# Performance work log

Measured on AMD Instinct MI355X. Metric: run time of the kernel, lower is better.

## Reference

```python
import jax, jax.numpy as jnp
import numpy as np

N_NODES = 100000
N_EDGES = 1600000
IN_CH, EDGE_DIM, HIDDEN, OUT_CH = 3, 3, 64, 1


def setup_inputs() -> dict:
    key = jax.random.key(0)
    ks = jax.random.split(key, 10)
    x = jax.random.normal(ks[0], (N_NODES, IN_CH), dtype=jnp.float32)
    edge_index = jax.random.randint(ks[1], (2, N_EDGES), 0, N_NODES, dtype=jnp.int64)
    edge_attr = jax.random.normal(ks[2], (N_EDGES, EDGE_DIM), dtype=jnp.float32)
    # Linear params (torch Linear: y = x @ W.T + b); we store W as (in, out)
    s1 = 1.0 / np.sqrt(IN_CH + EDGE_DIM)
    W1 = jax.random.uniform(ks[3], (IN_CH + EDGE_DIM, HIDDEN), jnp.float32, -s1, s1)
    b1 = jax.random.uniform(ks[4], (HIDDEN,), jnp.float32, -s1, s1)
    s2 = 1.0 / np.sqrt(HIDDEN + EDGE_DIM)
    W2 = jax.random.uniform(ks[5], (HIDDEN + EDGE_DIM, HIDDEN), jnp.float32, -s2, s2)
    b2 = jax.random.uniform(ks[6], (HIDDEN,), jnp.float32, -s2, s2)
    s3 = 1.0 / np.sqrt(HIDDEN)
    W3 = jax.random.uniform(ks[7], (HIDDEN, OUT_CH), jnp.float32, -s3, s3)
    b3 = jax.random.uniform(ks[8], (OUT_CH,), jnp.float32, -s3, s3)
    return {"x": x, "edge_index": edge_index, "edge_attr": edge_attr,
            "W1": W1, "b1": b1, "W2": W2, "b2": b2, "W3": W3, "b3": b3}


def _edge_conv(h, src, dst, edge_attr, W, b, n_nodes):
    # gather source node features, concat edge_attr, linear, scatter-add at dst
    msg = jnp.concatenate([h[src], edge_attr], axis=-1) @ W + b  # [E, out]
    return jax.ops.segment_sum(msg, dst, num_segments=n_nodes)   # [N, out]


def reference(x, edge_index, edge_attr, W1, b1, W2, b2, W3, b3):
    src, dst = edge_index[0], edge_index[1]  # PyG source_to_target: aggregate at edge_index[1]
    n = x.shape[0]
    h = jax.nn.relu(_edge_conv(x, src, dst, edge_attr, W1, b1, n))
    h = jax.nn.relu(_edge_conv(h, src, dst, edge_attr, W2, b2, n))
    return h @ W3 + b3  # (n_nodes, 1) anomaly logits
```

## Files before the change

kernel.cpp:

```cpp
#include <hip/hip_runtime.h>

#define N_NODES 100000
#define N_EDGES 1600000
#define NCHUNK 256
#define CHUNK_E (N_EDGES / NCHUNK)
#define BSHIFT 6
#define BMASK 63
#define NBUCK 1563
#define REC_CAP 1536


typedef unsigned int uint4_ev __attribute__((ext_vector_type(4)));
typedef short bf16x8 __attribute__((ext_vector_type(8)));
typedef float f32x4 __attribute__((ext_vector_type(4)));

__device__ __forceinline__ unsigned short f2bf(float f) {
    unsigned int u = __float_as_uint(f);
    unsigned int r = (u + 0x7fff + ((u >> 16) & 1)) >> 16;
    return (unsigned short)r;
}
__device__ __forceinline__ unsigned int pack2bf(float a, float b) {
    return (unsigned int)f2bf(a) | ((unsigned int)f2bf(b) << 16);
}
__device__ __forceinline__ float bflo(unsigned int v) { return __uint_as_float(v << 16); }
__device__ __forceinline__ float bfhi(unsigned int v) { return __uint_as_float(v & 0xffff0000u); }

__device__ __forceinline__ float4 nt_load4(const float4* p) {
    uint4_ev v = __builtin_nontemporal_load((const uint4_ev*)p);
    return make_float4(__uint_as_float(v.x), __uint_as_float(v.y),
                       __uint_as_float(v.z), __uint_as_float(v.w));
}

__device__ __forceinline__ int wave_incl_scan(int v, int lane) {
#pragma unroll
    for (int off = 1; off < 64; off <<= 1) {
        int t = __shfl_up(v, off, 64);
        if (lane >= off) v += t;
    }
    return v;
}

__global__ __launch_bounds__(1024) void k_hist(const int* __restrict__ ei,
                                               int* __restrict__ tbl,
                                               const float* __restrict__ W2,
                                               unsigned short* __restrict__ wpk,
                                               const float* __restrict__ x,
                                               float4* __restrict__ xp) {
    if (blockIdx.x > NCHUNK) {
        int i = (blockIdx.x - NCHUNK - 1) * 1024 + threadIdx.x;
        if (i < N_NODES)
            xp[i] = make_float4(x[i * 3 + 0], x[i * 3 + 1], x[i * 3 + 2], 0.f);
        return;
    }
    if (blockIdx.x == NCHUNK) {
        int i = threadIdx.x;
        if (i < 512) {
            int lane = i & 63, hh = (i >> 6) & 1, nt = i >> 7;
            int col = nt * 16 + (lane & 15);
            int k0 = hh * 32 + (lane >> 4) * 8;
#pragma unroll
            for (int j = 0; j < 8; j++)
                wpk[i * 8 + j] = f2bf(W2[(k0 + j) * 64 + col]);
        }
        return;
    }
    __shared__ int h[NBUCK];
    for (int i = threadIdx.x; i < NBUCK; i += 1024) h[i] = 0;
    __syncthreads();
    const int base = blockIdx.x * CHUNK_E;
    for (int i = threadIdx.x; i < CHUNK_E; i += 1024)
        atomicAdd(&h[ei[N_EDGES + base + i] >> BSHIFT], 1);
    __syncthreads();
    for (int i = threadIdx.x; i < NBUCK; i += 1024)
        tbl[blockIdx.x * NBUCK + i] = h[i];
}

__global__ __launch_bounds__(256) void k_colscan(int* __restrict__ tbl,
                                                 int* __restrict__ bsum) {
    const int b = blockIdx.x, t = threadIdx.x;
    int v = tbl[t * NBUCK + b];
    int lane = t & 63, w = t >> 6;
    int inc = wave_incl_scan(v, lane);
    __shared__ int ws[4];
    if (lane == 63) ws[w] = inc;
    __syncthreads();
    int wo = 0;
    for (int k = 0; k < w; k++) wo += ws[k];
    tbl[t * NBUCK + b] = wo + inc - v;
    if (t == 255) bsum[b] = wo + inc;
}

__global__ __launch_bounds__(1024) void k_basescan(const int* __restrict__ bsum,
                                                   int* __restrict__ bbase) {
    int t = threadIdx.x, lane = t & 63, w = t >> 6;
    int i0 = 2 * t, i1 = 2 * t + 1;
    int v0 = (i0 < NBUCK) ? bsum[i0] : 0;
    int v1 = (i1 < NBUCK) ? bsum[i1] : 0;
    int s = v0 + v1;
    int inc = wave_incl_scan(s, lane);
    __shared__ int ws[16];
    if (lane == 63) ws[w] = inc;
    __syncthreads();
    int wo = 0;
    for (int k = 0; k < w; k++) wo += ws[k];
    int excl = wo + inc - s;
    if (i0 < NBUCK) bbase[i0] = excl;
    if (i1 < NBUCK) bbase[i1] = excl + v0;
    if (i0 == NBUCK - 1) bbase[NBUCK] = excl + v0;
}

__global__ __launch_bounds__(1024) void k_scatter(const int* __restrict__ ei,
                                                  const float* __restrict__ ea,
                                                  const int* __restrict__ tbl,
                                                  const int* __restrict__ bbase,
                                                  float4* __restrict__ stg) {
    __shared__ int cur[NBUCK];
    for (int i = threadIdx.x; i < NBUCK; i += 1024)
        cur[i] = tbl[blockIdx.x * NBUCK + i] + bbase[i];
    __syncthreads();
    const int base = blockIdx.x * CHUNK_E;
    for (int i = threadIdx.x; i < CHUNK_E; i += 1024) {
        int e = base + i;
        int src = ei[e];
        int dst = ei[N_EDGES + e];
        float a0 = ea[(size_t)e * 3 + 0];
        float a1 = ea[(size_t)e * 3 + 1];
        float a2 = ea[(size_t)e * 3 + 2];
        int p = atomicAdd(&cur[dst >> BSHIFT], 1);
        unsigned pk = (unsigned)src | ((unsigned)(dst & BMASK) << 17);
        stg[p] = make_float4(__uint_as_float(pk), a0, a1, a2);
    }
}

__global__ __launch_bounds__(256) void k_finalize(
    const float4* __restrict__ stg, const int* __restrict__ bbase,
    const float4* __restrict__ xp, const float* __restrict__ W1,
    const float* __restrict__ b1, const float* __restrict__ W2,
    const float* __restrict__ b2, const bf16x8* __restrict__ wpk,
    int* __restrict__ csr, int* __restrict__ degp, int* __restrict__ rowend,
    unsigned int* __restrict__ zu, unsigned int* __restrict__ eu) {
    __shared__ float4 rec[REC_CAP];
    __shared__ int hist[64], lofs[64], cur[64];
    __shared__ float sU[64 * 3], sT[64 * 3];
    const int b = blockIdx.x, t = threadIdx.x;
    const int base = bbase[b], cnt = bbase[b + 1] - base;
    if (t < 64) hist[t] = 0;
    __syncthreads();
    const float* stgf = (const float*)stg;
    for (int i = t; i < cnt; i += 256) {
        unsigned pk = __float_as_uint(stgf[(size_t)(base + i) * 4]);
        atomicAdd(&hist[pk >> 17], 1);
    }
    __syncthreads();
    if (t < 64) {
        int v = hist[t];
        int inc = wave_incl_scan(v, t);
        lofs[t] = inc - v;
        cur[t] = inc - v;
    }
    __syncthreads();
    for (int i = t; i < cnt; i += 256) {
        float4 r = nt_load4(&stg[base + i]);
        unsigned pk = __float_as_uint(r.x);
        int p = atomicAdd(&cur[pk >> 17], 1);
        if (p < REC_CAP) rec[p] = r;
    }
    __syncthreads();
    {
        const int l = t >> 2, sub = t & 3;
        const int n = b * 64 + l;
        const int d = hist[l], lo = lofs[l];
        float u0 = 0, u1 = 0, u2 = 0, t0 = 0, t1 = 0, t2 = 0;
        for (int j = sub; j < d; j += 4) {
            float4 r = rec[lo + j];
            unsigned pk = __float_as_uint(r.x);
            int src = pk & 0x1FFFF;
            csr[base + lo + j] = src;
            t0 += r.y; t1 += r.z; t2 += r.w;
            float4 xv = xp[src];
            u0 += xv.x; u1 += xv.y; u2 += xv.z;
        }
#pragma unroll
        for (int off = 1; off <= 2; off <<= 1) {
            u0 += __shfl_xor(u0, off, 64); u1 += __shfl_xor(u1, off, 64);
            u2 += __shfl_xor(u2, off, 64); t0 += __shfl_xor(t0, off, 64);
            t1 += __shfl_xor(t1, off, 64); t2 += __shfl_xor(t2, off, 64);
        }
        if (sub == 0) {
            sU[l * 3 + 0] = u0; sU[l * 3 + 1] = u1; sU[l * 3 + 2] = u2;
            sT[l * 3 + 0] = t0; sT[l * 3 + 1] = t1; sT[l * 3 + 2] = t2;
            if (n < N_NODES) {
                degp[n] = d;
                rowend[n] = base + lo + d;
            }
        }
    }
    __syncthreads();
    const int lane = t & 63, w = t >> 6;
    const int tb = b * 64 + w * 16;
    if (tb >= N_NODES) return;
    const int col = lane & 15;
    const int q = lane >> 4;
    const int ln = w * 16 + col;
    const float d = (float)hist[ln];
    const float u0 = sU[ln * 3], u1 = sU[ln * 3 + 1], u2 = sU[ln * 3 + 2];
    const float t0 = sT[ln * 3], t1 = sT[ln * 3 + 1], t2 = sT[ln * 3 + 2];
    bf16x8 af[2];
#pragma unroll
    for (int h = 0; h < 2; h++) {
#pragma unroll
        for (int j = 0; j < 8; j++) {
            int c = h * 32 + q * 8 + j;
            float a = d * b1[c];
            a = fmaf(u0, W1[0 * 64 + c], a);
            a = fmaf(u1, W1[1 * 64 + c], a);
            a = fmaf(u2, W1[2 * 64 + c], a);
            a = fmaf(t0, W1[3 * 64 + c], a);
            a = fmaf(t1, W1[4 * 64 + c], a);
            a = fmaf(t2, W1[5 * 64 + c], a);
            af[h][j] = (short)f2bf(fmaxf(a, 0.f));
        }
    }
    f32x4 acc[4];
#pragma unroll
    for (int nt = 0; nt < 4; nt++) {
        bf16x8 b0 = wpk[(nt * 2 + 0) * 64 + lane];
        bf16x8 b1f = wpk[(nt * 2 + 1) * 64 + lane];
        f32x4 a = {0.f, 0.f, 0.f, 0.f};
        a = __builtin_amdgcn_mfma_f32_16x16x32_bf16(af[0], b0, a, 0, 0, 0);
        a = __builtin_amdgcn_mfma_f32_16x16x32_bf16(af[1], b1f, a, 0, 0, 0);
        acc[nt] = a;
    }
#pragma unroll
    for (int nt = 0; nt < 4; nt++) {
#pragma unroll
        for (int r = 0; r < 4; r++) {
            float v = acc[nt][r];
            float pv = __shfl_xor(v, 1, 64);
            if ((lane & 1) == 0) {
                int nr = tb + q * 4 + r;
                zu[(size_t)nr * 32 + nt * 8 + (col >> 1)] = pack2bf(v, pv);
            }
        }
    }
    const float eb = b2[lane];
    const float w64 = W2[64 * 64 + lane];
    const float w65 = W2[65 * 64 + lane];
    const float w66 = W2[66 * 64 + lane];
#pragma unroll 4
    for (int mm = 0; mm < 16; mm++) {
        int lm = w * 16 + mm;
        float dd = (float)hist[lm];
        float s0 = sT[lm * 3], s1 = sT[lm * 3 + 1], s2 = sT[lm * 3 + 2];
        float e = dd * eb;
        e = fmaf(s0, w64, e); e = fmaf(s1, w65, e); e = fmaf(s2, w66, e);
        float pe = __shfl_xor(e, 1, 64);
        if ((lane & 1) == 0)
            eu[(size_t)(tb + mm) * 32 + (lane >> 1)] = pack2bf(e, pe);
    }
}

__global__ __launch_bounds__(256) void k_agg(
    const unsigned int* __restrict__ zu, const unsigned int* __restrict__ eu,
    const int* __restrict__ rowend, const int* __restrict__ degp,
    const int* __restrict__ csr, const float* __restrict__ W3,
    const float* __restrict__ b3, float* __restrict__ out) {
    const int lane = threadIdx.x & 63;
    const int li = lane & 15;
    const int q = li & 7;
    const int r = li >> 3;
    const int n = blockIdx.x * 16 + (threadIdx.x >> 4);

    float cw3[8];
#pragma unroll
    for (int m = 0; m < 8; m++) cw3[m] = W3[8 * q + m];
    const float b3v = b3[0];

    const int end = rowend[n], d = degp[n], start = end - d;
    float S[8];
#pragma unroll
    for (int m = 0; m < 8; m++) S[m] = 0.f;

    for (int c = start; c < end; c += 16) {
        int idx[8];
        float mk[8];
        uint4 v[8];
#pragma unroll
        for (int u = 0; u < 8; u++) {
            int i = c + 2 * u + r;
            bool ok = i < end;
            mk[u] = ok ? 1.f : 0.f;
            idx[u] = csr[ok ? i : start];
        }
#pragma unroll
        for (int u = 0; u < 8; u++)
            v[u] = *(const uint4*)&zu[(size_t)idx[u] * 32 + q * 4];
#pragma unroll
        for (int u = 0; u < 8; u++) {
            S[0] = fmaf(mk[u], bflo(v[u].x), S[0]); S[1] = fmaf(mk[u], bfhi(v[u].x), S[1]);
            S[2] = fmaf(mk[u], bflo(v[u].y), S[2]); S[3] = fmaf(mk[u], bfhi(v[u].y), S[3]);
            S[4] = fmaf(mk[u], bflo(v[u].z), S[4]); S[5] = fmaf(mk[u], bfhi(v[u].z), S[5]);
            S[6] = fmaf(mk[u], bflo(v[u].w), S[6]); S[7] = fmaf(mk[u], bfhi(v[u].w), S[7]);
        }
    }
#pragma unroll
    for (int m = 0; m < 8; m++) S[m] += __shfl_xor(S[m], 8, 64);

    const uint4 ev = *(const uint4*)&eu[(size_t)n * 32 + q * 4];
    float contrib;
    {
        float h0 = fmaxf(S[0] + bflo(ev.x), 0.f);
        float h1v = fmaxf(S[1] + bfhi(ev.x), 0.f);
        float h2v = fmaxf(S[2] + bflo(ev.y), 0.f);
        float h3 = fmaxf(S[3] + bfhi(ev.y), 0.f);
        float h4 = fmaxf(S[4] + bflo(ev.z), 0.f);
        float h5 = fmaxf(S[5] + bfhi(ev.z), 0.f);
        float h6 = fmaxf(S[6] + bflo(ev.w), 0.f);
        float h7 = fmaxf(S[7] + bfhi(ev.w), 0.f);
        contrib = h0 * cw3[0];
        contrib = fmaf(h1v, cw3[1], contrib);
        contrib = fmaf(h2v, cw3[2], contrib);
        contrib = fmaf(h3, cw3[3], contrib);
        contrib = fmaf(h4, cw3[4], contrib);
        contrib = fmaf(h5, cw3[5], contrib);
        contrib = fmaf(h6, cw3[6], contrib);
        contrib = fmaf(h7, cw3[7], contrib);
    }
    contrib += __shfl_xor(contrib, 1, 64);
    contrib += __shfl_xor(contrib, 2, 64);
    contrib += __shfl_xor(contrib, 4, 64);
    if (li == 0) out[n] = contrib + b3v;
}

extern "C" void kernel_launch(void* const* d_in, const int* in_sizes, int n_in,
                              void* d_out, int out_size, void* d_ws, size_t ws_size,
                              hipStream_t stream) {
    const float* x  = (const float*)d_in[0];
    const int*   ei = (const int*)d_in[1];
    const float* ea = (const float*)d_in[2];
    const float* W1 = (const float*)d_in[3];
    const float* b1 = (const float*)d_in[4];
    const float* W2 = (const float*)d_in[5];
    const float* b2 = (const float*)d_in[6];
    const float* W3 = (const float*)d_in[7];
    const float* b3 = (const float*)d_in[8];
    float* out = (float*)d_out;

    char* ws = (char*)d_ws;
    int*    tbl    = (int*)(ws + 0);
    int*    bsum   = (int*)(ws + 1600512);
    int*    bbase  = (int*)(ws + 1606912);
    int*    degp   = (int*)(ws + 1613312);
    int*    rowend = (int*)(ws + 2013440);
    int*    csr    = (int*)(ws + 2413568);
    float4* stg    = (float4*)(ws + 8813568);
    unsigned int* zu = (unsigned int*)(ws + 34413568);
    unsigned int* eu = (unsigned int*)(ws + 47213568);
    unsigned short* wpk = (unsigned short*)(ws + 60013568);
    float4* xp = (float4*)(ws + 60021760);

    k_hist<<<NCHUNK + 99, 1024, 0, stream>>>(ei, tbl, W2, wpk, x, xp);
    k_colscan<<<NBUCK, 256, 0, stream>>>(tbl, bsum);
    k_basescan<<<1, 1024, 0, stream>>>(bsum, bbase);
    k_scatter<<<NCHUNK, 1024, 0, stream>>>(ei, ea, tbl, bbase, stg);
    k_finalize<<<NBUCK, 256, 0, stream>>>(stg, bbase, xp, W1, b1, W2, b2,
                                          (const bf16x8*)wpk, csr, degp, rowend, zu, eu);
    k_agg<<<N_NODES / 16, 256, 0, stream>>>(zu, eu, rowend, degp, csr, W3, b3, out);
}
```

Before: 187.4 us.

## Merge column and base scans via last-block pattern, halve chunks, prefetch staging

Fuses the per-bucket column scan and the global base scan into one kernel, where the last block to finish (found with an atomic counter and threadfence) computes the bucket bases. This removes one launch. The edge chunk count drops from 256 to 128, which shrinks the histogram table and the column scan width. k_finalize now loads staged records into registers once instead of reading them twice, and degree/rowend are replaced with a single rowptr array. The risks are a serialized tail in the last block and less parallelism in the hist and scatter kernels.

```diff
diff --git a/kernel.cpp b/kernel.cpp
--- a/kernel.cpp
+++ b/kernel.cpp
@@ -2,7 +2,7 @@
 
 #define N_NODES 100000
 #define N_EDGES 1600000
-#define NCHUNK 256
+#define NCHUNK 128
 #define CHUNK_E (N_EDGES / NCHUNK)
 #define BSHIFT 6
 #define BMASK 63
@@ -45,7 +45,8 @@
                                                const float* __restrict__ W2,
                                                unsigned short* __restrict__ wpk,
                                                const float* __restrict__ x,
-                                               float4* __restrict__ xp) {
+                                               float4* __restrict__ xp,
+                                               int* __restrict__ done) {
     if (blockIdx.x > NCHUNK) {
         int i = (blockIdx.x - NCHUNK - 1) * 1024 + threadIdx.x;
         if (i < N_NODES)
@@ -54,6 +55,7 @@
     }
     if (blockIdx.x == NCHUNK) {
         int i = threadIdx.x;
+        if (i == 0) *done = 0;
         if (i < 512) {
             int lane = i & 63, hh = (i >> 6) & 1, nt = i >> 7;
             int col = nt * 16 + (lane & 15);
@@ -75,38 +77,47 @@
         tbl[blockIdx.x * NBUCK + i] = h[i];
 }
 
-__global__ __launch_bounds__(256) void k_colscan(int* __restrict__ tbl,
-                                                 int* __restrict__ bsum) {
+__global__ __launch_bounds__(128) void k_scan(int* __restrict__ tbl,
+                                              int* __restrict__ bsum,
+                                              int* __restrict__ bbase,
+                                              int* __restrict__ done) {
     const int b = blockIdx.x, t = threadIdx.x;
+    const int lane = t & 63, w = t >> 6;
+    __shared__ int ws[2];
+    __shared__ int lastflag;
     int v = tbl[t * NBUCK + b];
-    int lane = t & 63, w = t >> 6;
     int inc = wave_incl_scan(v, lane);
-    __shared__ int ws[4];
     if (lane == 63) ws[w] = inc;
     __syncthreads();
-    int wo = 0;
-    for (int k = 0; k < w; k++) wo += ws[k];
-    tbl[t * NBUCK + b] = wo + inc - v;
-    if (t == 255) bsum[b] = wo + inc;
-}
-
-__global__ __launch_bounds__(1024) void k_basescan(const int* __restrict__ bsum,
-                                                   int* __restrict__ bbase) {
-    int t = threadIdx.x, lane = t & 63, w = t >> 6;
-    int i0 = 2 * t, i1 = 2 * t + 1;
-    int v0 = (i0 < NBUCK) ? bsum[i0] : 0;
-    int v1 = (i1 < NBUCK) ? bsum[i1] : 0;
-    int s = v0 + v1;
-    int inc = wave_incl_scan(s, lane);
-    __shared__ int ws[16];
-    if (lane == 63) ws[w] = inc;
-    __syncthreads();
-    int wo = 0;
-    for (int k = 0; k < w; k++) wo += ws[k];
-    int excl = wo + inc - s;
-    if (i0 < NBUCK) bbase[i0] = excl;
-    if (i1 < NBUCK) bbase[i1] = excl + v0;
-    if (i0 == NBUCK - 1) bbase[NBUCK] = excl + v0;
+    int excl = inc - v + (w ? ws[0] : 0);
+    tbl[t * NBUCK + b] = excl;
+    if (t == 127) bsum[b] = excl + v;
+    __threadfence();
+    __syncthreads();
+    if (t == 0) lastflag = (atomicAdd(done, 1) == NBUCK - 1);
+    __syncthreads();
+    if (!lastflag) return;
+    __threadfence();
+    int loc[13];
+    int s = 0;
+#pragma unroll
+    for (int k = 0; k < 13; k++) {
+        int i = t * 13 + k;
+        int x = (i < NBUCK) ? bsum[i] : 0;
+        loc[k] = s;
+        s += x;
+    }
+    int tot = s;
+    int incb = wave_incl_scan(tot, lane);
+    if (lane == 63) ws[w] = incb;
+    __syncthreads();
+    int basev = incb - tot + (w ? ws[0] : 0);
+#pragma unroll
+    for (int k = 0; k < 13; k++) {
+        int i = t * 13 + k;
+        if (i < NBUCK) bbase[i] = basev + loc[k];
+    }
+    if (t == 127) bbase[NBUCK] = basev + tot;
 }
 
 __global__ __launch_bounds__(1024) void k_scatter(const int* __restrict__ ei,
@@ -137,20 +148,28 @@
     const float4* __restrict__ xp, const float* __restrict__ W1,
     const float* __restrict__ b1, const float* __restrict__ W2,
     const float* __restrict__ b2, const bf16x8* __restrict__ wpk,
-    int* __restrict__ csr, int* __restrict__ degp, int* __restrict__ rowend,
+    int* __restrict__ csr, int* __restrict__ rowptr,
     unsigned int* __restrict__ zu, unsigned int* __restrict__ eu) {
     __shared__ float4 rec[REC_CAP];
     __shared__ int hist[64], lofs[64], cur[64];
     __shared__ float sU[64 * 3], sT[64 * 3];
     const int b = blockIdx.x, t = threadIdx.x;
     const int base = bbase[b], cnt = bbase[b + 1] - base;
+    float4 r_[6];
+#pragma unroll
+    for (int k = 0; k < 6; k++) {
+        int i = t + k * 256;
+        if (i < cnt) r_[k] = nt_load4(&stg[base + i]);
+    }
     if (t < 64) hist[t] = 0;
     __syncthreads();
-    const float* stgf = (const float*)stg;
-    for (int i = t; i < cnt; i += 256) {
-        unsigned pk = __float_as_uint(stgf[(size_t)(base + i) * 4]);
-        atomicAdd(&hist[pk >> 17], 1);
-    }
+#pragma unroll
+    for (int k = 0; k < 6; k++) {
+        int i = t + k * 256;
+        if (i < cnt) atomicAdd(&hist[__float_as_uint(r_[k].x) >> 17], 1);
+    }
+    for (int i = t + 6 * 256; i < cnt; i += 256)
+        atomicAdd(&hist[__float_as_uint(((const float*)stg)[(size_t)(base + i) * 4]) >> 17], 1);
     __syncthreads();
     if (t < 64) {
         int v = hist[t];
@@ -159,11 +178,13 @@
         cur[t] = inc - v;
     }
     __syncthreads();
-    for (int i = t; i < cnt; i += 256) {
-        float4 r = nt_load4(&stg[base + i]);
-        unsigned pk = __float_as_uint(r.x);
-        int p = atomicAdd(&cur[pk >> 17], 1);
-        if (p < REC_CAP) rec[p] = r;
+#pragma unroll
+    for (int k = 0; k < 6; k++) {
+        int i = t + k * 256;
+        if (i < cnt) {
+            int p = atomicAdd(&cur[__float_as_uint(r_[k].x) >> 17], 1);
+            if (p < REC_CAP) rec[p] = r_[k];
+        }
     }
     __syncthreads();
     {
@@ -190,8 +211,8 @@
             sU[l * 3 + 0] = u0; sU[l * 3 + 1] = u1; sU[l * 3 + 2] = u2;
             sT[l * 3 + 0] = t0; sT[l * 3 + 1] = t1; sT[l * 3 + 2] = t2;
             if (n < N_NODES) {
-                degp[n] = d;
-                rowend[n] = base + lo + d;
+                rowptr[n] = base + lo;
+                if (n == N_NODES - 1) rowptr[N_NODES] = base + lo + d;
             }
         }
     }
@@ -262,9 +283,9 @@
 
 __global__ __launch_bounds__(256) void k_agg(
     const unsigned int* __restrict__ zu, const unsigned int* __restrict__ eu,
-    const int* __restrict__ rowend, const int* __restrict__ degp,
-    const int* __restrict__ csr, const float* __restrict__ W3,
-    const float* __restrict__ b3, float* __restrict__ out) {
+    const int* __restrict__ rowptr, const int* __restrict__ csr,
+    const float* __restrict__ W3, const float* __restrict__ b3,
+    float* __restrict__ out) {
     const int lane = threadIdx.x & 63;
     const int li = lane & 15;
     const int q = li & 7;
@@ -276,7 +297,7 @@
     for (int m = 0; m < 8; m++) cw3[m] = W3[8 * q + m];
     const float b3v = b3[0];
 
-    const int end = rowend[n], d = degp[n], start = end - d;
+    const int start = rowptr[n], end = rowptr[n + 1];
     float S[8];
 #pragma unroll
     for (int m = 0; m < 8; m++) S[m] = 0.f;
@@ -348,22 +369,21 @@
 
     char* ws = (char*)d_ws;
     int*    tbl    = (int*)(ws + 0);
-    int*    bsum   = (int*)(ws + 1600512);
-    int*    bbase  = (int*)(ws + 1606912);
-    int*    degp   = (int*)(ws + 1613312);
-    int*    rowend = (int*)(ws + 2013440);
-    int*    csr    = (int*)(ws + 2413568);
-    float4* stg    = (float4*)(ws + 8813568);
-    unsigned int* zu = (unsigned int*)(ws + 34413568);
-    unsigned int* eu = (unsigned int*)(ws + 47213568);
-    unsigned short* wpk = (unsigned short*)(ws + 60013568);
-    float4* xp = (float4*)(ws + 60021760);
-
-    k_hist<<<NCHUNK + 99, 1024, 0, stream>>>(ei, tbl, W2, wpk, x, xp);
-    k_colscan<<<NBUCK, 256, 0, stream>>>(tbl, bsum);
-    k_basescan<<<1, 1024, 0, stream>>>(bsum, bbase);
+    int*    bsum   = (int*)(ws + 800256);
+    int*    bbase  = (int*)(ws + 806656);
+    int*    done   = (int*)(ws + 813056);
+    int*    rowptr = (int*)(ws + 813312);
+    int*    csr    = (int*)(ws + 1213440);
+    float4* stg    = (float4*)(ws + 7613440);
+    unsigned int* zu = (unsigned int*)(ws + 33213440);
+    unsigned int* eu = (unsigned int*)(ws + 46013440);
+    unsigned short* wpk = (unsigned short*)(ws + 58813440);
+    float4* xp = (float4*)(ws + 58821632);
+
+    k_hist<<<NCHUNK + 99, 1024, 0, stream>>>(ei, tbl, W2, wpk, x, xp, done);
+    k_scan<<<NBUCK, 128, 0, stream>>>(tbl, bsum, bbase, done);
     k_scatter<<<NCHUNK, 1024, 0, stream>>>(ei, ea, tbl, bbase, stg);
     k_finalize<<<NBUCK, 256, 0, stream>>>(stg, bbase, xp, W1, b1, W2, b2,
-                                          (const bf16x8*)wpk, csr, degp, rowend, zu, eu);
-    k_agg<<<N_NODES / 16, 256, 0, stream>>>(zu, eu, rowend, degp, csr, W3, b3, out);
-}
+                                          (const bf16x8*)wpk, csr, rowptr, zu, eu);
+    k_agg<<<N_NODES / 16, 256, 0, stream>>>(zu, eu, rowptr, csr, W3, b3, out);
+}
```

Result: slower. 286.0 us (+52.6%).
